# Optimization experiments

Measured on AMD Instinct MI355X. Metric: run time of the kernel, lower is better.

The kernel has to match this reference:

```python
import jax, jax.numpy as jnp
import numpy as np

N = 100000
E = 1600000
IN_DIM = 128
HID = 32
HEADS = 4
OUT_DIM = 64
NEG_SLOPE = 0.2  # PyG GATConv default LeakyReLU slope


def setup_inputs() -> dict:
    key = jax.random.key(0)
    ks = jax.random.split(key, 10)
    s = 1.0 / np.sqrt(IN_DIM)
    s2 = 1.0 / np.sqrt(HID * HEADS)
    return {
        "x": jax.random.normal(ks[0], (N, IN_DIM), dtype=jnp.float32),
        "edge_index": jax.random.randint(ks[1], (2, E), 0, N, dtype=jnp.int32),
        # layer 1: GATConv(128 -> 32, heads=4)
        "W1": jax.random.normal(ks[2], (IN_DIM, HEADS * HID), dtype=jnp.float32) * s,
        "a_src1": jax.random.normal(ks[3], (HEADS, HID), dtype=jnp.float32) * s,
        "a_dst1": jax.random.normal(ks[4], (HEADS, HID), dtype=jnp.float32) * s,
        "b1": jnp.zeros((HEADS * HID,), dtype=jnp.float32),
        # layer 2: GATConv(128 -> 64, heads=1)
        "W2": jax.random.normal(ks[5], (HEADS * HID, OUT_DIM), dtype=jnp.float32) * s2,
        "a_src2": jax.random.normal(ks[6], (1, OUT_DIM), dtype=jnp.float32) * s2,
        "a_dst2": jax.random.normal(ks[7], (1, OUT_DIM), dtype=jnp.float32) * s2,
        "b2": jnp.zeros((OUT_DIM,), dtype=jnp.float32),
    }


def _gat_conv(x, src, dst, W, a_src, a_dst, b, heads, out_c):
    # x: [N, F] -> h: [N, H, C]
    h = (x @ W).reshape(N, heads, out_c)
    alpha_src = jnp.sum(h * a_src, axis=-1)  # [N, H]
    alpha_dst = jnp.sum(h * a_dst, axis=-1)  # [N, H]
    # per-edge attention logits, softmax grouped by destination node
    e = jax.nn.leaky_relu(alpha_src[src] + alpha_dst[dst], NEG_SLOPE)  # [E', H]
    e_max = jax.ops.segment_max(e, dst, num_segments=N)[dst]
    e_exp = jnp.exp(e - e_max)
    denom = jax.ops.segment_sum(e_exp, dst, num_segments=N)[dst]
    alpha = e_exp / denom  # [E', H]
    msg = h[src] * alpha[..., None]  # [E', H, C]
    out = jax.ops.segment_sum(msg, dst, num_segments=N)  # [N, H, C]
    return out.reshape(N, heads * out_c) + b


def reference(x, edge_index, W1, a_src1, a_dst1, b1, W2, a_src2, a_dst2, b2):
    # PyG GATConv default add_self_loops=True
    loop = jnp.arange(N, dtype=edge_index.dtype)
    src = jnp.concatenate([edge_index[0], loop])
    dst = jnp.concatenate([edge_index[1], loop])
    h = _gat_conv(x, src, dst, W1, a_src1, a_dst1, b1, HEADS, HID)
    h = jax.nn.elu(h)  # dropout omitted (deterministic reference)
    out = _gat_conv(h, src, dst, W2, a_src2, a_dst2, b2, 1, OUT_DIM)
    return out
```

## Files before the change

### kernel.cpp

```cpp
#include <hip/hip_runtime.h>
#include <hip/hip_fp16.h>

#define NNODES 100000
#define NEDGES 1600000
#define INDIM 128
#define HID 32
#define HEADS 4
#define OUTDIM 64
#define NEG_SLOPE 0.2f
#define NRANGES 8
#define RSIZE (NNODES / NRANGES)

__device__ __forceinline__ float lrelu(float x) { return x > 0.f ? x : NEG_SLOPE * x; }

__global__ void k_degree(const int* __restrict__ dst, int* __restrict__ deg, int E) {
    int i = blockIdx.x * blockDim.x + threadIdx.x;
    if (i < E) atomicAdd(&deg[dst[i]], 1);
}

__global__ void k_scanA(const int* __restrict__ deg, int* __restrict__ rowptr,
                        int* __restrict__ bsum, int N) {
    __shared__ int ls[1024];
    int t = threadIdx.x;
    int i = blockIdx.x * 1024 + t;
    int v = (i < N) ? deg[i] : 0;
    ls[t] = v;
    __syncthreads();
    for (int off = 1; off < 1024; off <<= 1) {
        int add = (t >= off) ? ls[t - off] : 0;
        __syncthreads();
        ls[t] += add;
        __syncthreads();
    }
    int incl = ls[t];
    if (i < N) rowptr[i] = incl - v;
    if (t == 1023) bsum[blockIdx.x] = incl;
}

__global__ void k_scanB(const int* __restrict__ bsum, int* __restrict__ boff, int nb) {
    __shared__ int ls[128];
    int t = threadIdx.x;
    int v = (t < nb) ? bsum[t] : 0;
    ls[t] = v;
    __syncthreads();
    for (int off = 1; off < 128; off <<= 1) {
        int add = (t >= off) ? ls[t - off] : 0;
        __syncthreads();
        ls[t] += add;
        __syncthreads();
    }
    if (t < nb) boff[t] = ls[t] - v;
}

__global__ void k_scanC(int* __restrict__ rowptr, int* __restrict__ cursor,
                        const int* __restrict__ boff, int N, int E) {
    int t = threadIdx.x;
    int i = blockIdx.x * 1024 + t;
    if (i < N) {
        int r = rowptr[i] + boff[blockIdx.x];
        rowptr[i] = r;
        cursor[i] = r;
    }
    if (blockIdx.x == 0 && t == 0) rowptr[N] = E;
}

__global__ __launch_bounds__(256) void k_fill(const int* __restrict__ src,
                                              const int* __restrict__ dst,
                                              int* __restrict__ cursor,
                                              int* __restrict__ csr_src, int E) {
    int range = blockIdx.x & (NRANGES - 1);
    int chunk = blockIdx.x >> 3;
    int nchunks = gridDim.x >> 3;
    int lo = range * RSIZE;
    int hi = (range == NRANGES - 1) ? NNODES : lo + RSIZE;
    int per = (E + nchunks - 1) / nchunks;
    int beg = chunk * per;
    int end = min(E, beg + per);
    for (int i = beg + threadIdx.x; i < end; i += 256) {
        int d = dst[i];
        if (d >= lo && d < hi) {
            int slot = atomicAdd(&cursor[d], 1);
            csr_src[slot] = src[i];
        }
    }
}

__global__ __launch_bounds__(256) void k_gemm1(const float* __restrict__ x,
                                               const float* __restrict__ W,
                                               __half* __restrict__ h) {
    __shared__ float Ws[INDIM * 128];
    int t = threadIdx.x;
    const float4* W4 = (const float4*)W;
    float4* Ws4 = (float4*)Ws;
    #pragma unroll
    for (int i = t; i < INDIM * 128 / 4; i += 256) Ws4[i] = W4[i];
    __syncthreads();

    int cg = t & 31;
    int rg = t >> 5;
    int r0 = blockIdx.x * 64 + rg * 8;
    const float4* x4 = (const float4*)x;

    int ridx[8];
    #pragma unroll
    for (int rr = 0; rr < 8; ++rr) {
        int r = r0 + rr;
        ridx[rr] = r < NNODES ? r : NNODES - 1;
    }
    float4 acc[8];
    #pragma unroll
    for (int rr = 0; rr < 8; ++rr) acc[rr] = make_float4(0.f, 0.f, 0.f, 0.f);

    for (int k = 0; k < INDIM; k += 4) {
        float4 wv0 = Ws4[(k + 0) * 32 + cg];
        float4 wv1 = Ws4[(k + 1) * 32 + cg];
        float4 wv2 = Ws4[(k + 2) * 32 + cg];
        float4 wv3 = Ws4[(k + 3) * 32 + cg];
        #pragma unroll
        for (int rr = 0; rr < 8; ++rr) {
            float4 xv = x4[(size_t)ridx[rr] * 32 + (k >> 2)];
            acc[rr].x = fmaf(xv.x, wv0.x, fmaf(xv.y, wv1.x, fmaf(xv.z, wv2.x, fmaf(xv.w, wv3.x, acc[rr].x))));
            acc[rr].y = fmaf(xv.x, wv0.y, fmaf(xv.y, wv1.y, fmaf(xv.z, wv2.y, fmaf(xv.w, wv3.y, acc[rr].y))));
            acc[rr].z = fmaf(xv.x, wv0.z, fmaf(xv.y, wv1.z, fmaf(xv.z, wv2.z, fmaf(xv.w, wv3.z, acc[rr].z))));
            acc[rr].w = fmaf(xv.x, wv0.w, fmaf(xv.y, wv1.w, fmaf(xv.z, wv2.w, fmaf(xv.w, wv3.w, acc[rr].w))));
        }
    }
    #pragma unroll
    for (int rr = 0; rr < 8; ++rr) {
        int r = r0 + rr;
        if (r < NNODES) {
            union { __half2 h2[2]; uint2 u; } pk;
            pk.h2[0] = __floats2half2_rn(acc[rr].x, acc[rr].y);
            pk.h2[1] = __floats2half2_rn(acc[rr].z, acc[rr].w);
            ((uint2*)h)[(size_t)r * 32 + cg] = pk.u;
        }
    }
}

__global__ __launch_bounds__(256) void k_gemm2(const float* __restrict__ x,
                                               const float* __restrict__ W,
                                               __half* __restrict__ h) {
    __shared__ float Ws[128 * OUTDIM];
    int t = threadIdx.x;
    const float4* W4 = (const float4*)W;
    float4* Ws4 = (float4*)Ws;
    #pragma unroll
    for (int i = t; i < 128 * OUTDIM / 4; i += 256) Ws4[i] = W4[i];
    __syncthreads();

    int cg = t & 15;
    int rg = t >> 4;
    int r0 = blockIdx.x * 64 + rg * 4;
    const float4* x4 = (const float4*)x;

    int ridx[4];
    #pragma unroll
    for (int rr = 0; rr < 4; ++rr) {
        int r = r0 + rr;
        ridx[rr] = r < NNODES ? r : NNODES - 1;
    }
    float4 acc[4];
    #pragma unroll
    for (int rr = 0; rr < 4; ++rr) acc[rr] = make_float4(0.f, 0.f, 0.f, 0.f);

    for (int k = 0; k < 128; k += 4) {
        float4 wv0 = Ws4[(k + 0) * 16 + cg];
        float4 wv1 = Ws4[(k + 1) * 16 + cg];
        float4 wv2 = Ws4[(k + 2) * 16 + cg];
        float4 wv3 = Ws4[(k + 3) * 16 + cg];
        #pragma unroll
        for (int rr = 0; rr < 4; ++rr) {
            float4 xv = x4[(size_t)ridx[rr] * 32 + (k >> 2)];
            acc[rr].x = fmaf(xv.x, wv0.x, fmaf(xv.y, wv1.x, fmaf(xv.z, wv2.x, fmaf(xv.w, wv3.x, acc[rr].x))));
            acc[rr].y = fmaf(xv.x, wv0.y, fmaf(xv.y, wv1.y, fmaf(xv.z, wv2.y, fmaf(xv.w, wv3.y, acc[rr].y))));
            acc[rr].z = fmaf(xv.x, wv0.z, fmaf(xv.y, wv1.z, fmaf(xv.z, wv2.z, fmaf(xv.w, wv3.z, acc[rr].z))));
            acc[rr].w = fmaf(xv.x, wv0.w, fmaf(xv.y, wv1.w, fmaf(xv.z, wv2.w, fmaf(xv.w, wv3.w, acc[rr].w))));
        }
    }
    #pragma unroll
    for (int rr = 0; rr < 4; ++rr) {
        int r = r0 + rr;
        if (r < NNODES) {
            union { __half2 h2[2]; uint2 u; } pk;
            pk.h2[0] = __floats2half2_rn(acc[rr].x, acc[rr].y);
            pk.h2[1] = __floats2half2_rn(acc[rr].z, acc[rr].w);
            ((uint2*)h)[(size_t)r * 16 + cg] = pk.u;
        }
    }
}

__global__ void k_alpha1(const __half* __restrict__ h, const float* __restrict__ a_src,
                         const float* __restrict__ a_dst, float* __restrict__ asrc,
                         float* __restrict__ adst) {
    int t = threadIdx.x;
    int n = blockIdx.x * 4 + (t >> 6);
    if (n >= NNODES) return;
    int l = t & 63;
    int c0 = 2 * l;
    int head = l >> 4;
    float2 hv = __half22float2(((const __half2*)h)[(size_t)n * 64 + l]);
    int wi = head * HID + (c0 & 31);
    float ps = hv.x * a_src[wi] + hv.y * a_src[wi + 1];
    float pd = hv.x * a_dst[wi] + hv.y * a_dst[wi + 1];
    #pragma unroll
    for (int off = 1; off < 16; off <<= 1) {
        ps += __shfl_xor(ps, off, 16);
        pd += __shfl_xor(pd, off, 16);
    }
    if ((l & 15) == 0) {
        asrc[n * 4 + head] = ps;
        adst[n * 4 + head] = pd;
    }
}

__global__ void k_alpha2(const __half* __restrict__ h, const float* __restrict__ a_src,
                         const float* __restrict__ a_dst, float* __restrict__ asrc,
                         float* __restrict__ adst) {
    int t = threadIdx.x;
    int n = blockIdx.x * 4 + (t >> 6);
    if (n >= NNODES) return;
    int l = t & 63;
    float hv = __half2float(h[(size_t)n * 64 + l]);
    float ps = hv * a_src[l];
    float pd = hv * a_dst[l];
    #pragma unroll
    for (int off = 1; off < 64; off <<= 1) {
        ps += __shfl_xor(ps, off, 64);
        pd += __shfl_xor(pd, off, 64);
    }
    if (l == 0) {
        asrc[n] = ps;
        adst[n] = pd;
    }
}

__global__ __launch_bounds__(256) void k_agg1(const __half* __restrict__ h,
                                              const float* __restrict__ asrc,
                                              const float* __restrict__ adst,
                                              const int* __restrict__ rowptr,
                                              const int* __restrict__ csr_src,
                                              const float* __restrict__ b,
                                              float* __restrict__ out) {
    int t = threadIdx.x;
    int n = blockIdx.x * 4 + (t >> 6);
    if (n >= NNODES) return;
    int l = t & 63;
    int head = l >> 4;
    int c0 = 2 * l;
    const __half2* hh = (const __half2*)h;

    float adsth = adst[n * 4 + head];
    float w = __expf(lrelu(asrc[n * 4 + head] + adsth));
    float2 hv = __half22float2(hh[(size_t)n * 64 + l]);
    float dsum = w;
    float a0 = w * hv.x;
    float a1 = w * hv.y;

    int beg = rowptr[n];
    int end = rowptr[n + 1];
    int p = beg;
    for (; p + 8 <= end; p += 8) {
        int s[8];
        #pragma unroll
        for (int j = 0; j < 8; ++j) s[j] = __builtin_amdgcn_readfirstlane(csr_src[p + j]);
        float ww[8];
        #pragma unroll
        for (int j = 0; j < 8; ++j) ww[j] = __expf(lrelu(asrc[(size_t)s[j] * 4 + head] + adsth));
        float2 hx[8];
        #pragma unroll
        for (int j = 0; j < 8; ++j) hx[j] = __half22float2(hh[(size_t)s[j] * 64 + l]);
        #pragma unroll
        for (int j = 0; j < 8; ++j) {
            dsum += ww[j];
            a0 = fmaf(ww[j], hx[j].x, a0);
            a1 = fmaf(ww[j], hx[j].y, a1);
        }
    }
    for (; p < end; ++p) {
        int s = __builtin_amdgcn_readfirstlane(csr_src[p]);
        float ws = __expf(lrelu(asrc[(size_t)s * 4 + head] + adsth));
        float2 hs = __half22float2(hh[(size_t)s * 64 + l]);
        dsum += ws;
        a0 = fmaf(ws, hs.x, a0);
        a1 = fmaf(ws, hs.y, a1);
    }
    float inv = 1.0f / dsum;
    float r0 = a0 * inv + b[c0];
    float r1 = a1 * inv + b[c0 + 1];
    r0 = r0 > 0.f ? r0 : __expf(r0) - 1.f;
    r1 = r1 > 0.f ? r1 : __expf(r1) - 1.f;
    *(float2*)&out[(size_t)n * 128 + c0] = make_float2(r0, r1);
}

__global__ __launch_bounds__(256) void k_agg2(const __half* __restrict__ h,
                                              const float* __restrict__ asrc,
                                              const float* __restrict__ adst,
                                              const int* __restrict__ rowptr,
                                              const int* __restrict__ csr_src,
                                              const float* __restrict__ b,
                                              float* __restrict__ out) {
    int t = threadIdx.x;
    int n = blockIdx.x * 4 + (t >> 6);
    if (n >= NNODES) return;
    int l = t & 63;

    float adv = adst[n];
    float w = __expf(lrelu(asrc[n] + adv));
    float dsum = w;
    float acc = w * __half2float(h[(size_t)n * 64 + l]);

    int beg = rowptr[n];
    int end = rowptr[n + 1];
    int p = beg;
    for (; p + 8 <= end; p += 8) {
        int s[8];
        #pragma unroll
        for (int j = 0; j < 8; ++j) s[j] = __builtin_amdgcn_readfirstlane(csr_src[p + j]);
        float ww[8];
        #pragma unroll
        for (int j = 0; j < 8; ++j) ww[j] = __expf(lrelu(asrc[s[j]] + adv));
        float hx[8];
        #pragma unroll
        for (int j = 0; j < 8; ++j) hx[j] = __half2float(h[(size_t)s[j] * 64 + l]);
        #pragma unroll
        for (int j = 0; j < 8; ++j) {
            dsum += ww[j];
            acc = fmaf(ww[j], hx[j], acc);
        }
    }
    for (; p < end; ++p) {
        int s = __builtin_amdgcn_readfirstlane(csr_src[p]);
        float ws = __expf(lrelu(asrc[s] + adv));
        acc = fmaf(ws, __half2float(h[(size_t)s * 64 + l]), acc);
        dsum += ws;
    }
    out[(size_t)n * 64 + l] = acc / dsum + b[l];
}

extern "C" void kernel_launch(void* const* d_in, const int* in_sizes, int n_in,
                              void* d_out, int out_size, void* d_ws, size_t ws_size,
                              hipStream_t stream) {
    const float* x      = (const float*)d_in[0];
    const int*   ei     = (const int*)d_in[1];
    const float* W1     = (const float*)d_in[2];
    const float* a_src1 = (const float*)d_in[3];
    const float* a_dst1 = (const float*)d_in[4];
    const float* b1     = (const float*)d_in[5];
    const float* W2     = (const float*)d_in[6];
    const float* a_src2 = (const float*)d_in[7];
    const float* a_dst2 = (const float*)d_in[8];
    const float* b2     = (const float*)d_in[9];
    float* out = (float*)d_out;

    const int* src = ei;
    const int* dst = ei + NEDGES;

    char* ws = (char*)d_ws;
    size_t off = 0;
    auto alloc = [&](size_t bytes) {
        void* p = ws + off;
        off += (bytes + 255) & ~255ull;
        return p;
    };
    int* rowptr   = (int*)alloc((NNODES + 1) * sizeof(int));
    int* cursor   = (int*)alloc(NNODES * sizeof(int));
    int* csr_src  = (int*)alloc((size_t)NEDGES * sizeof(int));
    __half* h1h   = (__half*)alloc((size_t)NNODES * 128 * sizeof(__half));
    float* eluh   = (float*)alloc((size_t)NNODES * 128 * sizeof(float));
    float* asrc1  = (float*)alloc((size_t)NNODES * 4 * sizeof(float));
    float* adst1  = (float*)alloc((size_t)NNODES * 4 * sizeof(float));
    int* bsum     = (int*)alloc(128 * sizeof(int));
    int* boff     = (int*)alloc(129 * sizeof(int));

    int nb = (NNODES + 1023) / 1024;

    hipMemsetAsync(cursor, 0, NNODES * sizeof(int), stream);
    k_degree<<<(NEDGES + 255) / 256, 256, 0, stream>>>(dst, cursor, NEDGES);
    k_scanA<<<nb, 1024, 0, stream>>>(cursor, rowptr, bsum, NNODES);
    k_scanB<<<1, 128, 0, stream>>>(bsum, boff, nb);
    k_scanC<<<nb, 1024, 0, stream>>>(rowptr, cursor, boff, NNODES, NEDGES);
    k_fill<<<NRANGES * 200, 256, 0, stream>>>(src, dst, cursor, csr_src, NEDGES);

    int gn = (NNODES + 3) / 4;

    k_gemm1<<<(NNODES + 63) / 64, 256, 0, stream>>>(x, W1, h1h);
    k_alpha1<<<gn, 256, 0, stream>>>(h1h, a_src1, a_dst1, asrc1, adst1);
    k_agg1<<<gn, 256, 0, stream>>>(h1h, asrc1, adst1, rowptr, csr_src, b1, eluh);

    k_gemm2<<<(NNODES + 63) / 64, 256, 0, stream>>>(eluh, W2, h1h);
    k_alpha2<<<gn, 256, 0, stream>>>(h1h, a_src2, a_dst2, asrc1, adst1);
    k_agg2<<<gn, 256, 0, stream>>>(h1h, asrc1, adst1, rowptr, csr_src, b2, out);
}
```

Baseline: 437.4 us.

## Precompute per-edge attention weights and halve GEMM shared-memory W tiles

Adds per-layer edge-weight kernels that compute exp(leaky_relu(asrc[s]+adst[n])) once per edge and store it as fp16 in CSR order. The aggregation kernels then read these weights instead of gathering asrc and evaluating exp inline, which was done redundantly across the lanes of each wavefront. Separately, both GEMMs now stage W through shared memory in two halves, which halves LDS use and could raise occupancy. The cost is an extra kernel launch and an extra write and read of the edge-weight buffer per layer, plus an fp16 rounding of the weights.

```diff
diff --git a/kernel.cpp b/kernel.cpp
--- a/kernel.cpp
+++ b/kernel.cpp
@@ -88,13 +88,10 @@
 __global__ __launch_bounds__(256) void k_gemm1(const float* __restrict__ x,
                                                const float* __restrict__ W,
                                                __half* __restrict__ h) {
-    __shared__ float Ws[INDIM * 128];
+    __shared__ float Ws[64 * 128];
     int t = threadIdx.x;
     const float4* W4 = (const float4*)W;
     float4* Ws4 = (float4*)Ws;
-    #pragma unroll
-    for (int i = t; i < INDIM * 128 / 4; i += 256) Ws4[i] = W4[i];
-    __syncthreads();
 
     int cg = t & 31;
     int rg = t >> 5;
@@ -111,19 +108,26 @@
     #pragma unroll
     for (int rr = 0; rr < 8; ++rr) acc[rr] = make_float4(0.f, 0.f, 0.f, 0.f);
 
-    for (int k = 0; k < INDIM; k += 4) {
-        float4 wv0 = Ws4[(k + 0) * 32 + cg];
-        float4 wv1 = Ws4[(k + 1) * 32 + cg];
-        float4 wv2 = Ws4[(k + 2) * 32 + cg];
-        float4 wv3 = Ws4[(k + 3) * 32 + cg];
-        #pragma unroll
-        for (int rr = 0; rr < 8; ++rr) {
-            float4 xv = x4[(size_t)ridx[rr] * 32 + (k >> 2)];
-            acc[rr].x = fmaf(xv.x, wv0.x, fmaf(xv.y, wv1.x, fmaf(xv.z, wv2.x, fmaf(xv.w, wv3.x, acc[rr].x))));
-            acc[rr].y = fmaf(xv.x, wv0.y, fmaf(xv.y, wv1.y, fmaf(xv.z, wv2.y, fmaf(xv.w, wv3.y, acc[rr].y))));
-            acc[rr].z = fmaf(xv.x, wv0.z, fmaf(xv.y, wv1.z, fmaf(xv.z, wv2.z, fmaf(xv.w, wv3.z, acc[rr].z))));
-            acc[rr].w = fmaf(xv.x, wv0.w, fmaf(xv.y, wv1.w, fmaf(xv.z, wv2.w, fmaf(xv.w, wv3.w, acc[rr].w))));
-        }
+    for (int half = 0; half < 2; ++half) {
+        #pragma unroll
+        for (int i = t; i < 64 * 128 / 4; i += 256) Ws4[i] = W4[half * (64 * 128 / 4) + i];
+        __syncthreads();
+        for (int k = 0; k < 64; k += 4) {
+            float4 wv0 = Ws4[(k + 0) * 32 + cg];
+            float4 wv1 = Ws4[(k + 1) * 32 + cg];
+            float4 wv2 = Ws4[(k + 2) * 32 + cg];
+            float4 wv3 = Ws4[(k + 3) * 32 + cg];
+            int kg = (half * 64 + k) >> 2;
+            #pragma unroll
+            for (int rr = 0; rr < 8; ++rr) {
+                float4 xv = x4[(size_t)ridx[rr] * 32 + kg];
+                acc[rr].x = fmaf(xv.x, wv0.x, fmaf(xv.y, wv1.x, fmaf(xv.z, wv2.x, fmaf(xv.w, wv3.x, acc[rr].x))));
+                acc[rr].y = fmaf(xv.x, wv0.y, fmaf(xv.y, wv1.y, fmaf(xv.z, wv2.y, fmaf(xv.w, wv3.y, acc[rr].y))));
+                acc[rr].z = fmaf(xv.x, wv0.z, fmaf(xv.y, wv1.z, fmaf(xv.z, wv2.z, fmaf(xv.w, wv3.z, acc[rr].z))));
+                acc[rr].w = fmaf(xv.x, wv0.w, fmaf(xv.y, wv1.w, fmaf(xv.z, wv2.w, fmaf(xv.w, wv3.w, acc[rr].w))));
+            }
+        }
+        __syncthreads();
     }
     #pragma unroll
     for (int rr = 0; rr < 8; ++rr) {
@@ -140,13 +144,10 @@
 __global__ __launch_bounds__(256) void k_gemm2(const float* __restrict__ x,
                                                const float* __restrict__ W,
                                                __half* __restrict__ h) {
-    __shared__ float Ws[128 * OUTDIM];
+    __shared__ float Ws[64 * OUTDIM];
     int t = threadIdx.x;
     const float4* W4 = (const float4*)W;
     float4* Ws4 = (float4*)Ws;
-    #pragma unroll
-    for (int i = t; i < 128 * OUTDIM / 4; i += 256) Ws4[i] = W4[i];
-    __syncthreads();
 
     int cg = t & 15;
     int rg = t >> 4;
@@ -163,19 +164,26 @@
     #pragma unroll
     for (int rr = 0; rr < 4; ++rr) acc[rr] = make_float4(0.f, 0.f, 0.f, 0.f);
 
-    for (int k = 0; k < 128; k += 4) {
-        float4 wv0 = Ws4[(k + 0) * 16 + cg];
-        float4 wv1 = Ws4[(k + 1) * 16 + cg];
-        float4 wv2 = Ws4[(k + 2) * 16 + cg];
-        float4 wv3 = Ws4[(k + 3) * 16 + cg];
-        #pragma unroll
-        for (int rr = 0; rr < 4; ++rr) {
-            float4 xv = x4[(size_t)ridx[rr] * 32 + (k >> 2)];
-            acc[rr].x = fmaf(xv.x, wv0.x, fmaf(xv.y, wv1.x, fmaf(xv.z, wv2.x, fmaf(xv.w, wv3.x, acc[rr].x))));
-            acc[rr].y = fmaf(xv.x, wv0.y, fmaf(xv.y, wv1.y, fmaf(xv.z, wv2.y, fmaf(xv.w, wv3.y, acc[rr].y))));
-            acc[rr].z = fmaf(xv.x, wv0.z, fmaf(xv.y, wv1.z, fmaf(xv.z, wv2.z, fmaf(xv.w, wv3.z, acc[rr].z))));
-            acc[rr].w = fmaf(xv.x, wv0.w, fmaf(xv.y, wv1.w, fmaf(xv.z, wv2.w, fmaf(xv.w, wv3.w, acc[rr].w))));
-        }
+    for (int half = 0; half < 2; ++half) {
+        #pragma unroll
+        for (int i = t; i < 64 * OUTDIM / 4; i += 256) Ws4[i] = W4[half * (64 * OUTDIM / 4) + i];
+        __syncthreads();
+        for (int k = 0; k < 64; k += 4) {
+            float4 wv0 = Ws4[(k + 0) * 16 + cg];
+            float4 wv1 = Ws4[(k + 1) * 16 + cg];
+            float4 wv2 = Ws4[(k + 2) * 16 + cg];
+            float4 wv3 = Ws4[(k + 3) * 16 + cg];
+            int kg = (half * 64 + k) >> 2;
+            #pragma unroll
+            for (int rr = 0; rr < 4; ++rr) {
+                float4 xv = x4[(size_t)ridx[rr] * 32 + kg];
+                acc[rr].x = fmaf(xv.x, wv0.x, fmaf(xv.y, wv1.x, fmaf(xv.z, wv2.x, fmaf(xv.w, wv3.x, acc[rr].x))));
+                acc[rr].y = fmaf(xv.x, wv0.y, fmaf(xv.y, wv1.y, fmaf(xv.z, wv2.y, fmaf(xv.w, wv3.y, acc[rr].y))));
+                acc[rr].z = fmaf(xv.x, wv0.z, fmaf(xv.y, wv1.z, fmaf(xv.z, wv2.z, fmaf(xv.w, wv3.z, acc[rr].z))));
+                acc[rr].w = fmaf(xv.x, wv0.w, fmaf(xv.y, wv1.w, fmaf(xv.z, wv2.w, fmaf(xv.w, wv3.w, acc[rr].w))));
+            }
+        }
+        __syncthreads();
     }
     #pragma unroll
     for (int rr = 0; rr < 4; ++rr) {
@@ -234,11 +242,55 @@
     }
 }
 
+__global__ __launch_bounds__(256) void k_edgew1(const int* __restrict__ rowptr,
+                                                const int* __restrict__ csr_src,
+                                                const float* __restrict__ asrc,
+                                                const float* __restrict__ adst,
+                                                __half* __restrict__ w) {
+    int t = threadIdx.x;
+    int n = blockIdx.x * 4 + (t >> 6);
+    if (n >= NNODES) return;
+    int l = t & 63;
+    int head = l & 3;
+    float ad = adst[n * 4 + head];
+    int beg = rowptr[n], end = rowptr[n + 1];
+    for (int p0 = beg; p0 < end; p0 += 16) {
+        int e = p0 + (l >> 2);
+        if (e < end) {
+            int s = csr_src[e];
+            float v = __expf(lrelu(asrc[(size_t)s * 4 + head] + ad));
+            w[(size_t)e * 4 + head] = __float2half(v);
+        }
+    }
+}
+
+__global__ __launch_bounds__(256) void k_edgew2(const int* __restrict__ rowptr,
+                                                const int* __restrict__ csr_src,
+                                                const float* __restrict__ asrc,
+                                                const float* __restrict__ adst,
+                                                __half* __restrict__ w) {
+    int t = threadIdx.x;
+    int n = blockIdx.x * 4 + (t >> 6);
+    if (n >= NNODES) return;
+    int l = t & 63;
+    float ad = adst[n];
+    int beg = rowptr[n], end = rowptr[n + 1];
+    for (int p0 = beg; p0 < end; p0 += 64) {
+        int e = p0 + l;
+        if (e < end) {
+            int s = csr_src[e];
+            w[e] = __float2half(__expf(lrelu(asrc[s] + ad)));
+        }
+    }
+}
+
+template <bool USEW>
 __global__ __launch_bounds__(256) void k_agg1(const __half* __restrict__ h,
                                               const float* __restrict__ asrc,
                                               const float* __restrict__ adst,
                                               const int* __restrict__ rowptr,
                                               const int* __restrict__ csr_src,
+                                              const __half* __restrict__ wbuf,
                                               const float* __restrict__ b,
                                               float* __restrict__ out) {
     int t = threadIdx.x;
@@ -265,7 +317,10 @@
         for (int j = 0; j < 8; ++j) s[j] = __builtin_amdgcn_readfirstlane(csr_src[p + j]);
         float ww[8];
         #pragma unroll
-        for (int j = 0; j < 8; ++j) ww[j] = __expf(lrelu(asrc[(size_t)s[j] * 4 + head] + adsth));
+        for (int j = 0; j < 8; ++j) {
+            if constexpr (USEW) ww[j] = __half2float(wbuf[(size_t)(p + j) * 4 + head]);
+            else ww[j] = __expf(lrelu(asrc[(size_t)s[j] * 4 + head] + adsth));
+        }
         float2 hx[8];
         #pragma unroll
         for (int j = 0; j < 8; ++j) hx[j] = __half22float2(hh[(size_t)s[j] * 64 + l]);
@@ -278,7 +333,9 @@
     }
     for (; p < end; ++p) {
         int s = __builtin_amdgcn_readfirstlane(csr_src[p]);
-        float ws = __expf(lrelu(asrc[(size_t)s * 4 + head] + adsth));
+        float ws;
+        if constexpr (USEW) ws = __half2float(wbuf[(size_t)p * 4 + head]);
+        else ws = __expf(lrelu(asrc[(size_t)s * 4 + head] + adsth));
         float2 hs = __half22float2(hh[(size_t)s * 64 + l]);
         dsum += ws;
         a0 = fmaf(ws, hs.x, a0);
@@ -292,11 +349,13 @@
     *(float2*)&out[(size_t)n * 128 + c0] = make_float2(r0, r1);
 }
 
+template <bool USEW>
 __global__ __launch_bounds__(256) void k_agg2(const __half* __restrict__ h,
                                               const float* __restrict__ asrc,
                                               const float* __restrict__ adst,
                                               const int* __restrict__ rowptr,
                                               const int* __restrict__ csr_src,
+                                              const __half* __restrict__ wbuf,
                                               const float* __restrict__ b,
                                               float* __restrict__ out) {
     int t = threadIdx.x;
@@ -318,7 +377,10 @@
         for (int j = 0; j < 8; ++j) s[j] = __builtin_amdgcn_readfirstlane(csr_src[p + j]);
         float ww[8];
         #pragma unroll
-        for (int j = 0; j < 8; ++j) ww[j] = __expf(lrelu(asrc[s[j]] + adv));
+        for (int j = 0; j < 8; ++j) {
+            if constexpr (USEW) ww[j] = __half2float(wbuf[p + j]);
+            else ww[j] = __expf(lrelu(asrc[s[j]] + adv));
+        }
         float hx[8];
         #pragma unroll
         for (int j = 0; j < 8; ++j) hx[j] = __half2float(h[(size_t)s[j] * 64 + l]);
@@ -330,7 +392,9 @@
     }
     for (; p < end; ++p) {
         int s = __builtin_amdgcn_readfirstlane(csr_src[p]);
-        float ws = __expf(lrelu(asrc[s] + adv));
+        float ws;
+        if constexpr (USEW) ws = __half2float(wbuf[p]);
+        else ws = __expf(lrelu(asrc[s] + adv));
         acc = fmaf(ws, __half2float(h[(size_t)s * 64 + l]), acc);
         dsum += ws;
     }
@@ -371,6 +435,8 @@
     float* adst1  = (float*)alloc((size_t)NNODES * 4 * sizeof(float));
     int* bsum     = (int*)alloc(128 * sizeof(int));
     int* boff     = (int*)alloc(129 * sizeof(int));
+    __half* wbuf  = (__half*)alloc((size_t)NEDGES * 4 * sizeof(__half));
+    const bool use_w = (off <= ws_size);
 
     int nb = (NNODES + 1023) / 1024;
 
@@ -385,9 +451,19 @@
 
     k_gemm1<<<(NNODES + 63) / 64, 256, 0, stream>>>(x, W1, h1h);
     k_alpha1<<<gn, 256, 0, stream>>>(h1h, a_src1, a_dst1, asrc1, adst1);
-    k_agg1<<<gn, 256, 0, stream>>>(h1h, asrc1, adst1, rowptr, csr_src, b1, eluh);
+    if (use_w) {
+        k_edgew1<<<gn, 256, 0, stream>>>(rowptr, csr_src, asrc1, adst1, wbuf);
+        k_agg1<true><<<gn, 256, 0, stream>>>(h1h, asrc1, adst1, rowptr, csr_src, wbuf, b1, eluh);
+    } else {
+        k_agg1<false><<<gn, 256, 0, stream>>>(h1h, asrc1, adst1, rowptr, csr_src, wbuf, b1, eluh);
+    }
 
     k_gemm2<<<(NNODES + 63) / 64, 256, 0, stream>>>(eluh, W2, h1h);
     k_alpha2<<<gn, 256, 0, stream>>>(h1h, a_src2, a_dst2, asrc1, adst1);
-    k_agg2<<<gn, 256, 0, stream>>>(h1h, asrc1, adst1, rowptr, csr_src, b2, out);
-}
+    if (use_w) {
+        k_edgew2<<<gn, 256, 0, stream>>>(rowptr, csr_src, asrc1, adst1, wbuf);
+        k_agg2<true><<<gn, 256, 0, stream>>>(h1h, asrc1, adst1, rowptr, csr_src, wbuf, b2, out);
+    } else {
+        k_agg2<false><<<gn, 256, 0, stream>>>(h1h, asrc1, adst1, rowptr, csr_src, wbuf, b2, out);
+    }
+}
```

Result: slower. 469.4 us (+7.3%).
